# Performance work log

Hardware: AMD Instinct MI355X
Metric: run time of the kernel (lower is better)

The kernel has to match this reference:

```python
import jax, jax.numpy as jnp
import numpy as np
import math

D_MODEL = 1024
H = 16
D_K = D_MODEL // H
SEQ = 4096
NEG = -1000000000.0  # mask constant from the original code


def setup_inputs() -> dict:
    key = jax.random.key(0)
    ks = jax.random.split(key, 7)
    return {
        "Q": jax.random.normal(ks[0], (SEQ, D_MODEL), dtype=jnp.float32),
        "K": jax.random.normal(ks[1], (SEQ, D_MODEL), dtype=jnp.float32),
        "V": jax.random.normal(ks[2], (SEQ, D_MODEL), dtype=jnp.float32),
        "W_Q": jax.random.normal(ks[3], (H, D_MODEL, D_K), dtype=jnp.float32),
        "W_K": jax.random.normal(ks[4], (H, D_MODEL, D_K), dtype=jnp.float32),
        "W_V": jax.random.normal(ks[5], (H, D_MODEL, D_K), dtype=jnp.float32),
        "W_O": jax.random.normal(ks[6], (D_MODEL, D_MODEL), dtype=jnp.float32),
        "mask": 1,
    }


def reference(Q, K, V, W_Q, W_K, W_V, W_O, mask):
    d_k = W_Q.shape[-1]
    s = Q.shape[0]
    # batched per-head projections: [h, s, d_k]
    Qh = jnp.einsum("sd,hdk->hsk", Q, W_Q)
    Kh = jnp.einsum("sd,hdk->hsk", K, W_K)
    Vh = jnp.einsum("sd,hdk->hsk", V, W_V)
    # scores: [h, s_q, s_k]
    scores = jnp.einsum("hqk,hsk->hqs", Qh, Kh) / math.sqrt(d_k)
    if mask:
        # faithful to torch: tril(scores) + triu(ones, 1) * -1e9
        lower = jnp.tril(jnp.ones((s, s), dtype=scores.dtype))
        upper = jnp.triu(jnp.ones((s, s), dtype=scores.dtype), k=1)
        scores = scores * lower + upper * NEG
    attn = jax.nn.softmax(scores, axis=-1)
    heads = jnp.einsum("hqs,hsk->hqk", attn, Vh)  # [h, s, d_k]
    # concat heads along feature dim in head order -> [s, h*d_k]
    concat = jnp.transpose(heads, (1, 0, 2)).reshape(s, -1)
    return concat @ W_O
```

## Files before the change

### kernel.cpp

```cpp
#include <hip/hip_runtime.h>
#include <hip/hip_bf16.h>

constexpr int S      = 4096;
constexpr int DMODEL = 1024;
constexpr int H      = 16;
constexpr int DK     = 64;

typedef __attribute__((ext_vector_type(8))) short          short8;
typedef __attribute__((ext_vector_type(4))) short          short4v;
typedef __attribute__((ext_vector_type(4))) float          float4v;
typedef __attribute__((ext_vector_type(4))) unsigned short ushort4v;
typedef __attribute__((ext_vector_type(8))) unsigned short ushort8;

__device__ __forceinline__ unsigned short f2bf(float x) {
    unsigned u = __builtin_bit_cast(unsigned, x);
    u += 0x7FFFu + ((u >> 16) & 1u);
    return (unsigned short)(u >> 16);
}
__device__ __forceinline__ float bf2f(unsigned short h) {
    unsigned u = ((unsigned)h) << 16;
    return __builtin_bit_cast(float, u);
}
__device__ __forceinline__ float fexp2(float x) { return __builtin_amdgcn_exp2f(x); }

__device__ __forceinline__ void gl_lds16(const unsigned short* g, unsigned short* l) {
    __builtin_amdgcn_global_load_lds(
        (const __attribute__((address_space(1))) unsigned int*)g,
        (__attribute__((address_space(3))) unsigned int*)l, 16, 0, 0);
}

__global__ __launch_bounds__(256) void prep_all(
    const float* __restrict__ Q, const float* __restrict__ K,
    const float* __restrict__ V,
    const float* __restrict__ WQ, const float* __restrict__ WK,
    const float* __restrict__ WV, const float* __restrict__ WO,
    unsigned short* __restrict__ QH, unsigned short* __restrict__ QL,
    unsigned short* __restrict__ KH, unsigned short* __restrict__ KL,
    unsigned short* __restrict__ Vb,
    unsigned short* __restrict__ WqtH, unsigned short* __restrict__ WqtL,
    unsigned short* __restrict__ WktH, unsigned short* __restrict__ WktL,
    unsigned short* __restrict__ Wvt,  unsigned short* __restrict__ WOt)
{
    const int zb = blockIdx.z;
    const int t  = threadIdx.x;

    if (zb < 3) {
        const size_t base = ((size_t)blockIdx.x * 256 + t) * 8;
        const float* src = (zb == 0) ? Q : (zb == 1) ? K : V;
        const float4 a = *(const float4*)(src + base);
        const float4 b = *(const float4*)(src + base + 4);
        const float xs[8] = {a.x, a.y, a.z, a.w, b.x, b.y, b.z, b.w};
        ushort8 hv, lv;
#pragma unroll
        for (int j = 0; j < 8; ++j) {
            const unsigned short h = f2bf(xs[j]);
            hv[j] = h;
            lv[j] = f2bf(xs[j] - bf2f(h));
        }
        if (zb == 0)      { *(ushort8*)(QH + base) = hv; *(ushort8*)(QL + base) = lv; }
        else if (zb == 1) { *(ushort8*)(KH + base) = hv; *(ushort8*)(KL + base) = lv; }
        else              { *(ushort8*)(Vb + base) = hv; }
        return;
    }

    const int bb = blockIdx.x;
    if (bb >= 1024) return;
    const int zfull = bb >> 4;
    const int which = zfull >> 4;
    const int z     = zfull & 15;
    const int r0    = (bb & 15) * 64;

    __shared__ float Ts[64][65];

    const float* in;
    unsigned short *oh, *ol;
    int z_mult, rstride;
    if (which == 0)      { in = WQ; oh = WqtH; ol = WqtL; z_mult = 65536; rstride = 64; }
    else if (which == 1) { in = WK; oh = WktH; ol = WktL; z_mult = 65536; rstride = 64; }
    else if (which == 2) { in = WV; oh = Wvt;  ol = nullptr; z_mult = 65536; rstride = 64; }
    else                 { in = WO; oh = WOt;  ol = nullptr; z_mult = 64;    rstride = 1024; }

    const float* src = in + (size_t)z * z_mult;
#pragma unroll
    for (int i = 0; i < 4; ++i) {
        const int row = (t >> 4) + i * 16;
        const int col = (t & 15) * 4;
        const float4 v = *(const float4*)&src[(size_t)(r0 + row) * rstride + col];
        Ts[row][col + 0] = v.x; Ts[row][col + 1] = v.y;
        Ts[row][col + 2] = v.z; Ts[row][col + 3] = v.w;
    }
    __syncthreads();
#pragma unroll
    for (int i = 0; i < 4; ++i) {
        const int c  = (t >> 4) + i * 16;
        const int rb = (t & 15) * 4;
        ushort4v hv, lv;
#pragma unroll
        for (int j = 0; j < 4; ++j) {
            const float x = Ts[rb + j][c];
            const unsigned short h = f2bf(x);
            hv[j] = h;
            lv[j] = f2bf(x - bf2f(h));
        }
        const size_t o = (size_t)(z * 64 + c) * 1024 + r0 + rb;
        *(ushort4v*)&oh[o] = hv;
        if (ol) *(ushort4v*)&ol[o] = lv;
    }
}

template <bool SPLIT, int EPI>
__device__ __forceinline__ void gemm_core(unsigned short* __restrict__ sm,
                                          const unsigned short* __restrict__ Ah,
                                          const unsigned short* __restrict__ Al,
                                          const unsigned short* __restrict__ Bh,
                                          const unsigned short* __restrict__ Bl,
                                          float* __restrict__ C,
                                          unsigned short* __restrict__ O1,
                                          unsigned short* __restrict__ O2,
                                          int m0, int n0)
{
    unsigned short* AsH = sm;
    unsigned short* BsH = sm + 4096;
    unsigned short* AsL = sm + 8192;
    unsigned short* BsL = sm + 12288;

    const int t    = threadIdx.x;
    const int wave = t >> 6;
    const int lane = t & 63;
    const int quad = lane >> 4;
    const int l15  = lane & 15;
    const int wm   = (wave & 1) * 64;
    const int wn   = (wave >> 1) * 64;

    float4v acc[4][4];
#pragma unroll
    for (int mi = 0; mi < 4; ++mi)
#pragma unroll
        for (int ni = 0; ni < 4; ++ni)
#pragma unroll
            for (int r = 0; r < 4; ++r) acc[mi][ni][r] = 0.f;

    for (int k0 = 0; k0 < 1024; k0 += 32) {
        __syncthreads();
#pragma unroll
        for (int i = 0; i < 2; ++i) {
            const int c   = t + 256 * i;
            const int row = c >> 2;
            const int kc  = (c & 3) * 8;
            const int lb  = (i * 256 + wave * 64) * 8;
            gl_lds16(&Ah[(size_t)(m0 + row) * 1024 + k0 + kc], AsH + lb);
            gl_lds16(&Bh[(size_t)(n0 + row) * 1024 + k0 + kc], BsH + lb);
            if (SPLIT) {
                gl_lds16(&Al[(size_t)(m0 + row) * 1024 + k0 + kc], AsL + lb);
                gl_lds16(&Bl[(size_t)(n0 + row) * 1024 + k0 + kc], BsL + lb);
            }
        }
        __syncthreads();

        short8 afh[4], bfh[4], afl[4], bfl[4];
#pragma unroll
        for (int mi = 0; mi < 4; ++mi)
            afh[mi] = *(const short8*)&AsH[(wm + mi * 16 + l15) * 32 + quad * 8];
#pragma unroll
        for (int ni = 0; ni < 4; ++ni)
            bfh[ni] = *(const short8*)&BsH[(wn + ni * 16 + l15) * 32 + quad * 8];
        if (SPLIT) {
#pragma unroll
            for (int mi = 0; mi < 4; ++mi)
                afl[mi] = *(const short8*)&AsL[(wm + mi * 16 + l15) * 32 + quad * 8];
#pragma unroll
            for (int ni = 0; ni < 4; ++ni)
                bfl[ni] = *(const short8*)&BsL[(wn + ni * 16 + l15) * 32 + quad * 8];
        }

#pragma unroll
        for (int mi = 0; mi < 4; ++mi)
#pragma unroll
            for (int ni = 0; ni < 4; ++ni) {
                acc[mi][ni] = __builtin_amdgcn_mfma_f32_16x16x32_bf16(
                    afh[mi], bfh[ni], acc[mi][ni], 0, 0, 0);
                if (SPLIT) {
                    acc[mi][ni] = __builtin_amdgcn_mfma_f32_16x16x32_bf16(
                        afh[mi], bfl[ni], acc[mi][ni], 0, 0, 0);
                    acc[mi][ni] = __builtin_amdgcn_mfma_f32_16x16x32_bf16(
                        afl[mi], bfh[ni], acc[mi][ni], 0, 0, 0);
                }
            }
    }

    if (EPI == 2) {
        __syncthreads();
        unsigned short* Ts = sm;
#pragma unroll
        for (int mi = 0; mi < 4; ++mi)
#pragma unroll
            for (int ni = 0; ni < 4; ++ni) {
                ushort4v pk;
#pragma unroll
                for (int r = 0; r < 4; ++r) pk[r] = f2bf(acc[mi][ni][r]);
                *(ushort4v*)&Ts[(wn + ni * 16 + l15) * 136 + wm + mi * 16 + quad * 4] = pk;
            }
        __syncthreads();
#pragma unroll
        for (int p = 0; p < 8; ++p) {
            const int n = p * 16 + (t >> 4);
            const int m = (t & 15) * 8;
            *(ushort8*)&O1[(size_t)(n0 + n) * 4096 + m0 + m] =
                *(const ushort8*)&Ts[n * 136 + m];
        }
        return;
    }

#pragma unroll
    for (int mi = 0; mi < 4; ++mi)
#pragma unroll
        for (int r = 0; r < 4; ++r) {
            const int m = m0 + wm + mi * 16 + quad * 4 + r;
            if (EPI == 0) {
                float* cp = C + (size_t)m * 1024 + n0 + wn + l15;
#pragma unroll
                for (int ni = 0; ni < 4; ++ni) cp[ni * 16] = acc[mi][ni][r];
            } else {
                unsigned short* o1 = O1 + (size_t)m * 1024 + n0 + wn + l15;
                unsigned short* o2 = O2 + (size_t)m * 1024 + n0 + wn + l15;
#pragma unroll
                for (int ni = 0; ni < 4; ++ni) {
                    const float v = acc[mi][ni][r];
                    const unsigned short hh = f2bf(v);
                    o1[ni * 16] = hh;
                    o2[ni * 16] = f2bf(v - bf2f(hh));
                }
            }
        }
}

__global__ __launch_bounds__(256) void proj_mfma(
    const unsigned short* __restrict__ XqH, const unsigned short* __restrict__ XqL,
    const unsigned short* __restrict__ XkH, const unsigned short* __restrict__ XkL,
    const unsigned short* __restrict__ Xv,
    const unsigned short* __restrict__ WqtH, const unsigned short* __restrict__ WqtL,
    const unsigned short* __restrict__ WktH, const unsigned short* __restrict__ WktL,
    const unsigned short* __restrict__ Wvt,
    float* __restrict__ Qc,
    unsigned short* __restrict__ KHg, unsigned short* __restrict__ KLg,
    unsigned short* __restrict__ Vt)
{
    __shared__ __align__(16) unsigned short smem[17408];
    const int m0 = blockIdx.x * 128, n0 = blockIdx.y * 128;
    if (blockIdx.z == 0)
        gemm_core<true, 0>(smem, XqH, XqL, WqtH, WqtL, Qc, nullptr, nullptr, m0, n0);
    else if (blockIdx.z == 1)
        gemm_core<true, 1>(smem, XkH, XkL, WktH, WktL, nullptr, KHg, KLg, m0, n0);
    else
        gemm_core<false, 2>(smem, Xv, nullptr, Wvt, nullptr, nullptr, Vt, nullptr, m0, n0);
}

__global__ __launch_bounds__(256) void out_gemm_mfma(
    const unsigned short* __restrict__ Ocb,
    const unsigned short* __restrict__ WOt,
    float* __restrict__ out)
{
    __shared__ __align__(16) unsigned short smem[2 * 4096];
    gemm_core<false, 0>(smem, Ocb, nullptr, WOt, nullptr, out, nullptr, nullptr,
                        blockIdx.x * 128, blockIdx.y * 128);
}

__global__ __launch_bounds__(512) void attn_mfma(const float* __restrict__ Qc,
                                                 const unsigned short* __restrict__ KHg,
                                                 const unsigned short* __restrict__ KLg,
                                                 const unsigned short* __restrict__ Vtg,
                                                 unsigned short* __restrict__ Ocb)
{
    __shared__ __align__(16) short Khi[64][72];
    __shared__ __align__(16) short Klo[64][72];
    __shared__ __align__(16) short Vts[64][72];
    __shared__ __align__(16) short Pb[8][16][72];

    const int bid = blockIdx.x;
    const int h   = bid & 15;
    const int g   = bid >> 4;
    const int qb  = (g < 16) ? (31 - g) : (g - 16);
    const int q0  = qb * 128;
    const int jtmax = 2 * qb + 1;

    const int t    = threadIdx.x;
    const int wave = t >> 6;
    const int lane = t & 63;
    const int quad = lane >> 4;
    const int l15  = lane & 15;

    constexpr float SCL = 0.18033688011112042f;

    short8 qhi[2], qlo[2];
    {
        const int qrow = q0 + wave * 16 + l15;
        const float* qp = Qc + (size_t)qrow * DMODEL + h * 64 + quad * 8;
#pragma unroll
        for (int ks = 0; ks < 2; ++ks) {
            float4 a = *(const float4*)(qp + ks * 32);
            float4 b = *(const float4*)(qp + ks * 32 + 4);
            const float xs[8] = {a.x, a.y, a.z, a.w, b.x, b.y, b.z, b.w};
#pragma unroll
            for (int j = 0; j < 8; ++j) {
                const unsigned short hi = f2bf(xs[j]);
                const unsigned short lo = f2bf(xs[j] - bf2f(hi));
                qhi[ks][j] = (short)hi;
                qlo[ks][j] = (short)lo;
            }
        }
    }

    short8 bones;
    {
        const short ob = (l15 == 0) ? (short)0x3F80 : (short)0;
#pragma unroll
        for (int j = 0; j < 8; ++j) bones[j] = ob;
    }

    float m_r[4] = {-1e30f, -1e30f, -1e30f, -1e30f};
    float4v lacc;
    float4v oacc[4];
#pragma unroll
    for (int r = 0; r < 4; ++r) lacc[r] = 0.f;
#pragma unroll
    for (int nt = 0; nt < 4; ++nt)
#pragma unroll
        for (int r = 0; r < 4; ++r) oacc[nt][r] = 0.f;

    const int srow = t >> 3;
    const int soff = (t & 7) * 8;

    ushort8 kh, kl, vt;
    kh = *(const ushort8*)&KHg[(size_t)srow * 1024 + h * 64 + soff];
    kl = *(const ushort8*)&KLg[(size_t)srow * 1024 + h * 64 + soff];
    vt = *(const ushort8*)&Vtg[(size_t)(h * 64 + srow) * 4096 + soff];

    for (int jt = 0; jt <= jtmax; ++jt) {
        const int j0 = jt * 64;
        *(ushort8*)&Khi[srow][soff] = kh;
        *(ushort8*)&Klo[srow][soff] = kl;
        *(ushort8*)&Vts[srow][soff] = vt;
        __syncthreads();

        if (jt < jtmax) {
            const int jn = j0 + 64;
            kh = *(const ushort8*)&KHg[(size_t)(jn + srow) * 1024 + h * 64 + soff];
            kl = *(const ushort8*)&KLg[(size_t)(jn + srow) * 1024 + h * 64 + soff];
            vt = *(const ushort8*)&Vtg[(size_t)(h * 64 + srow) * 4096 + jn + soff];
        }

        float4v sacc[4];
#pragma unroll
        for (int nt = 0; nt < 4; ++nt)
#pragma unroll
            for (int r = 0; r < 4; ++r) sacc[nt][r] = 0.f;
#pragma unroll
        for (int nt = 0; nt < 4; ++nt) {
            const int key = nt * 16 + l15;
#pragma unroll
            for (int ks = 0; ks < 2; ++ks) {
                const short8 bh = *(const short8*)&Khi[key][ks * 32 + quad * 8];
                const short8 bl = *(const short8*)&Klo[key][ks * 32 + quad * 8];
                sacc[nt] = __builtin_amdgcn_mfma_f32_16x16x32_bf16(qhi[ks], bh, sacc[nt], 0, 0, 0);
                sacc[nt] = __builtin_amdgcn_mfma_f32_16x16x32_bf16(qhi[ks], bl, sacc[nt], 0, 0, 0);
                sacc[nt] = __builtin_amdgcn_mfma_f32_16x16x32_bf16(qlo[ks], bh, sacc[nt], 0, 0, 0);
            }
        }

        if (j0 + 63 > q0 + wave * 16) {
#pragma unroll
            for (int nt = 0; nt < 4; ++nt) {
                const int jg = j0 + nt * 16 + l15;
#pragma unroll
                for (int r = 0; r < 4; ++r) {
                    const int qg = q0 + wave * 16 + quad * 4 + r;
                    const float v = sacc[nt][r] * SCL;
                    sacc[nt][r] = (jg > qg) ? -1e9f : v;
                }
            }
        } else {
#pragma unroll
            for (int nt = 0; nt < 4; ++nt)
#pragma unroll
                for (int r = 0; r < 4; ++r)
                    sacc[nt][r] *= SCL;
        }

        float rmax[4];
#pragma unroll
        for (int r = 0; r < 4; ++r)
            rmax[r] = fmaxf(fmaxf(sacc[0][r], sacc[1][r]), fmaxf(sacc[2][r], sacc[3][r]));
#pragma unroll
        for (int off = 1; off < 16; off <<= 1)
#pragma unroll
            for (int r = 0; r < 4; ++r)
                rmax[r] = fmaxf(rmax[r], __shfl_xor(rmax[r], off));

        float alpha[4];
#pragma unroll
        for (int r = 0; r < 4; ++r) {
            const float mn = fmaxf(m_r[r], rmax[r]);
            alpha[r] = fexp2(m_r[r] - mn);
            m_r[r] = mn;
        }

#pragma unroll
        for (int nt = 0; nt < 4; ++nt)
#pragma unroll
            for (int r = 0; r < 4; ++r)
                sacc[nt][r] = fexp2(sacc[nt][r] - m_r[r]);

#pragma unroll
        for (int r = 0; r < 4; ++r) lacc[r] *= alpha[r];
#pragma unroll
        for (int nt = 0; nt < 4; ++nt)
#pragma unroll
            for (int r = 0; r < 4; ++r)
                oacc[nt][r] *= alpha[r];

#pragma unroll
        for (int nt = 0; nt < 4; ++nt)
#pragma unroll
            for (int r = 0; r < 4; ++r)
                Pb[wave][quad * 4 + r][nt * 16 + l15] = (short)f2bf(sacc[nt][r]);
        __asm__ volatile("s_waitcnt lgkmcnt(0)" ::: "memory");

        short8 af[2];
        af[0] = *(const short8*)&Pb[wave][l15][quad * 8];
        af[1] = *(const short8*)&Pb[wave][l15][32 + quad * 8];
#pragma unroll
        for (int nt = 0; nt < 4; ++nt) {
            const int dk = nt * 16 + l15;
#pragma unroll
            for (int ks = 0; ks < 2; ++ks) {
                const short8 bv = *(const short8*)&Vts[dk][ks * 32 + quad * 8];
                oacc[nt] = __builtin_amdgcn_mfma_f32_16x16x32_bf16(af[ks], bv, oacc[nt], 0, 0, 0);
            }
        }
        lacc = __builtin_amdgcn_mfma_f32_16x16x32_bf16(af[0], bones, lacc, 0, 0, 0);
        lacc = __builtin_amdgcn_mfma_f32_16x16x32_bf16(af[1], bones, lacc, 0, 0, 0);
        __syncthreads();
    }

#pragma unroll
    for (int r = 0; r < 4; ++r) {
        const float lsum = __shfl(lacc[r], (lane & 48));
        const float inv  = 1.0f / lsum;
        const int qg = q0 + wave * 16 + quad * 4 + r;
        unsigned short* op = Ocb + (size_t)qg * DMODEL + h * 64 + l15;
#pragma unroll
        for (int nt = 0; nt < 4; ++nt)
            op[nt * 16] = f2bf(oacc[nt][r] * inv);
    }
}

extern "C" void kernel_launch(void* const* d_in, const int* in_sizes, int n_in,
                              void* d_out, int out_size, void* d_ws, size_t ws_size,
                              hipStream_t stream)
{
    const float* Q  = (const float*)d_in[0];
    const float* K  = (const float*)d_in[1];
    const float* V  = (const float*)d_in[2];
    const float* WQ = (const float*)d_in[3];
    const float* WK = (const float*)d_in[4];
    const float* WV = (const float*)d_in[5];
    const float* WO = (const float*)d_in[6];

    float* out = (float*)d_out;

    const size_t SD4 = (size_t)S * DMODEL * 4;
    const size_t SD2 = (size_t)S * DMODEL * 2;
    const size_t W2  = (size_t)DMODEL * DMODEL * 2;
    char* p = (char*)d_ws;
    auto take = [&](size_t b) { char* r = p; p += b; return r; };

    float* Qc = (float*)take(SD4);
    unsigned short* KHg = (unsigned short*)take(SD2);
    unsigned short* KLg = (unsigned short*)take(SD2);
    unsigned short* Vtg = (unsigned short*)take(SD2);
    unsigned short* XqH = (unsigned short*)take(SD2);
    unsigned short* XqL = (unsigned short*)take(SD2);
    unsigned short* XkH = (unsigned short*)take(SD2);
    unsigned short* XkL = (unsigned short*)take(SD2);
    unsigned short* Xv  = (unsigned short*)take(SD2);
    unsigned short* WqtH = (unsigned short*)take(W2);
    unsigned short* WqtL = (unsigned short*)take(W2);
    unsigned short* WktH = (unsigned short*)take(W2);
    unsigned short* WktL = (unsigned short*)take(W2);
    unsigned short* Wvt  = (unsigned short*)take(W2);
    unsigned short* WOt  = (unsigned short*)take(W2);
    unsigned short* Ocb  = (unsigned short*)take(SD2);

    prep_all<<<dim3(2048, 1, 4), 256, 0, stream>>>(
        Q, K, V, WQ, WK, WV, WO,
        XqH, XqL, XkH, XkL, Xv, WqtH, WqtL, WktH, WktL, Wvt, WOt);
    proj_mfma<<<dim3(S / 128, DMODEL / 128, 3), 256, 0, stream>>>(
        XqH, XqL, XkH, XkL, Xv, WqtH, WqtL, WktH, WktL, Wvt, Qc, KHg, KLg, Vtg);
    attn_mfma<<<dim3((S / 128) * H), 512, 0, stream>>>(Qc, KHg, KLg, Vtg, Ocb);
    out_gemm_mfma<<<dim3(S / 128, DMODEL / 128), 256, 0, stream>>>(Ocb, WOt, out);
}
```

Measured before the change: 332.9 us.

## Skip fully-masked key tiles per wave and defer softmax rescale in attention

Each wave now skips all QK, softmax and PV work for key tiles lying entirely above its 16 query rows, keeping only the shared LDS staging and barriers. Scaling is folded into an fma inside exp2, so the max is taken on unscaled scores. The online-softmax rescale of the accumulators is skipped when no row's max grows anywhere in the wave. P is packed with the hardware v_cvt_pk_bf16_f32 instruction instead of software rounding. This cuts wasted MFMA and exp work on the causal diagonal, at the cost of more wave divergence and a slightly different mask constant.

```diff
diff --git a/kernel.cpp b/kernel.cpp
--- a/kernel.cpp
+++ b/kernel.cpp
@@ -22,6 +22,12 @@
     return __builtin_bit_cast(float, u);
 }
 __device__ __forceinline__ float fexp2(float x) { return __builtin_amdgcn_exp2f(x); }
+
+__device__ __forceinline__ unsigned cvtpk_bf16(float lo, float hi) {
+    unsigned r;
+    asm("v_cvt_pk_bf16_f32 %0, %1, %2" : "=v"(r) : "v"(lo), "v"(hi));
+    return r;
+}
 
 __device__ __forceinline__ void gl_lds16(const unsigned short* g, unsigned short* l) {
     __builtin_amdgcn_global_load_lds(
@@ -335,6 +341,7 @@
     kl = *(const ushort8*)&KLg[(size_t)srow * 1024 + h * 64 + soff];
     vt = *(const ushort8*)&Vtg[(size_t)(h * 64 + srow) * 4096 + soff];
 
+    const int qrow_lo = q0 + wave * 16;
     for (int jt = 0; jt <= jtmax; ++jt) {
         const int j0 = jt * 64;
         *(ushort8*)&Khi[srow][soff] = kh;
@@ -349,96 +356,97 @@
             vt = *(const ushort8*)&Vtg[(size_t)(h * 64 + srow) * 4096 + jn + soff];
         }
 
-        float4v sacc[4];
-#pragma unroll
-        for (int nt = 0; nt < 4; ++nt)
-#pragma unroll
-            for (int r = 0; r < 4; ++r) sacc[nt][r] = 0.f;
-#pragma unroll
-        for (int nt = 0; nt < 4; ++nt) {
-            const int key = nt * 16 + l15;
-#pragma unroll
-            for (int ks = 0; ks < 2; ++ks) {
-                const short8 bh = *(const short8*)&Khi[key][ks * 32 + quad * 8];
-                const short8 bl = *(const short8*)&Klo[key][ks * 32 + quad * 8];
-                sacc[nt] = __builtin_amdgcn_mfma_f32_16x16x32_bf16(qhi[ks], bh, sacc[nt], 0, 0, 0);
-                sacc[nt] = __builtin_amdgcn_mfma_f32_16x16x32_bf16(qhi[ks], bl, sacc[nt], 0, 0, 0);
-                sacc[nt] = __builtin_amdgcn_mfma_f32_16x16x32_bf16(qlo[ks], bh, sacc[nt], 0, 0, 0);
-            }
-        }
-
-        if (j0 + 63 > q0 + wave * 16) {
+        if (j0 <= qrow_lo + 15) {
+            float4v sacc[4];
+#pragma unroll
+            for (int nt = 0; nt < 4; ++nt)
+#pragma unroll
+                for (int r = 0; r < 4; ++r) sacc[nt][r] = 0.f;
 #pragma unroll
             for (int nt = 0; nt < 4; ++nt) {
-                const int jg = j0 + nt * 16 + l15;
+                const int key = nt * 16 + l15;
+#pragma unroll
+                for (int ks = 0; ks < 2; ++ks) {
+                    const short8 bh = *(const short8*)&Khi[key][ks * 32 + quad * 8];
+                    const short8 bl = *(const short8*)&Klo[key][ks * 32 + quad * 8];
+                    sacc[nt] = __builtin_amdgcn_mfma_f32_16x16x32_bf16(qhi[ks], bh, sacc[nt], 0, 0, 0);
+                    sacc[nt] = __builtin_amdgcn_mfma_f32_16x16x32_bf16(qhi[ks], bl, sacc[nt], 0, 0, 0);
+                    sacc[nt] = __builtin_amdgcn_mfma_f32_16x16x32_bf16(qlo[ks], bh, sacc[nt], 0, 0, 0);
+                }
+            }
+
+            if (j0 + 63 > qrow_lo) {
+#pragma unroll
+                for (int nt = 0; nt < 4; ++nt) {
+                    const int jg = j0 + nt * 16 + l15;
+#pragma unroll
+                    for (int r = 0; r < 4; ++r) {
+                        const int qg = qrow_lo + quad * 4 + r;
+                        if (jg > qg) sacc[nt][r] = -1e10f;
+                    }
+                }
+            }
+
+            float rmax[4];
+#pragma unroll
+            for (int r = 0; r < 4; ++r)
+                rmax[r] = fmaxf(fmaxf(sacc[0][r], sacc[1][r]), fmaxf(sacc[2][r], sacc[3][r]));
+#pragma unroll
+            for (int off = 1; off < 16; off <<= 1)
+#pragma unroll
+                for (int r = 0; r < 4; ++r)
+                    rmax[r] = fmaxf(rmax[r], __shfl_xor(rmax[r], off));
+
+            float rs[4];
+#pragma unroll
+            for (int r = 0; r < 4; ++r) rs[r] = rmax[r] * SCL;
+            const bool grow = (rs[0] > m_r[0]) || (rs[1] > m_r[1]) ||
+                              (rs[2] > m_r[2]) || (rs[3] > m_r[3]);
+            if (__any(grow)) {
 #pragma unroll
                 for (int r = 0; r < 4; ++r) {
-                    const int qg = q0 + wave * 16 + quad * 4 + r;
-                    const float v = sacc[nt][r] * SCL;
-                    sacc[nt][r] = (jg > qg) ? -1e9f : v;
-                }
-            }
-        } else {
+                    const float mn   = fmaxf(m_r[r], rs[r]);
+                    const float alpha = fexp2(m_r[r] - mn);
+                    m_r[r] = mn;
+                    lacc[r] *= alpha;
+#pragma unroll
+                    for (int nt = 0; nt < 4; ++nt) oacc[nt][r] *= alpha;
+                }
+            }
+
 #pragma unroll
             for (int nt = 0; nt < 4; ++nt)
 #pragma unroll
                 for (int r = 0; r < 4; ++r)
-                    sacc[nt][r] *= SCL;
-        }
-
-        float rmax[4];
-#pragma unroll
-        for (int r = 0; r < 4; ++r)
-            rmax[r] = fmaxf(fmaxf(sacc[0][r], sacc[1][r]), fmaxf(sacc[2][r], sacc[3][r]));
-#pragma unroll
-        for (int off = 1; off < 16; off <<= 1)
-#pragma unroll
-            for (int r = 0; r < 4; ++r)
-                rmax[r] = fmaxf(rmax[r], __shfl_xor(rmax[r], off));
-
-        float alpha[4];
-#pragma unroll
-        for (int r = 0; r < 4; ++r) {
-            const float mn = fmaxf(m_r[r], rmax[r]);
-            alpha[r] = fexp2(m_r[r] - mn);
-            m_r[r] = mn;
-        }
-
-#pragma unroll
-        for (int nt = 0; nt < 4; ++nt)
-#pragma unroll
-            for (int r = 0; r < 4; ++r)
-                sacc[nt][r] = fexp2(sacc[nt][r] - m_r[r]);
-
-#pragma unroll
-        for (int r = 0; r < 4; ++r) lacc[r] *= alpha[r];
-#pragma unroll
-        for (int nt = 0; nt < 4; ++nt)
-#pragma unroll
-            for (int r = 0; r < 4; ++r)
-                oacc[nt][r] *= alpha[r];
-
-#pragma unroll
-        for (int nt = 0; nt < 4; ++nt)
-#pragma unroll
-            for (int r = 0; r < 4; ++r)
-                Pb[wave][quad * 4 + r][nt * 16 + l15] = (short)f2bf(sacc[nt][r]);
-        __asm__ volatile("s_waitcnt lgkmcnt(0)" ::: "memory");
-
-        short8 af[2];
-        af[0] = *(const short8*)&Pb[wave][l15][quad * 8];
-        af[1] = *(const short8*)&Pb[wave][l15][32 + quad * 8];
-#pragma unroll
-        for (int nt = 0; nt < 4; ++nt) {
-            const int dk = nt * 16 + l15;
-#pragma unroll
-            for (int ks = 0; ks < 2; ++ks) {
-                const short8 bv = *(const short8*)&Vts[dk][ks * 32 + quad * 8];
-                oacc[nt] = __builtin_amdgcn_mfma_f32_16x16x32_bf16(af[ks], bv, oacc[nt], 0, 0, 0);
-            }
-        }
-        lacc = __builtin_amdgcn_mfma_f32_16x16x32_bf16(af[0], bones, lacc, 0, 0, 0);
-        lacc = __builtin_amdgcn_mfma_f32_16x16x32_bf16(af[1], bones, lacc, 0, 0, 0);
+                    sacc[nt][r] = fexp2(__builtin_fmaf(sacc[nt][r], SCL, -m_r[r]));
+
+#pragma unroll
+            for (int r = 0; r < 4; ++r) {
+                const int prow = quad * 4 + r;
+#pragma unroll
+                for (int np = 0; np < 2; ++np) {
+                    const unsigned w = cvtpk_bf16(sacc[2 * np][r], sacc[2 * np + 1][r]);
+                    Pb[wave][prow][(2 * np) * 16 + l15]     = (short)(w & 0xffffu);
+                    Pb[wave][prow][(2 * np + 1) * 16 + l15] = (short)(w >> 16);
+                }
+            }
+            __asm__ volatile("s_waitcnt lgkmcnt(0)" ::: "memory");
+
+            short8 af[2];
+            af[0] = *(const short8*)&Pb[wave][l15][quad * 8];
+            af[1] = *(const short8*)&Pb[wave][l15][32 + quad * 8];
+#pragma unroll
+            for (int nt = 0; nt < 4; ++nt) {
+                const int dk = nt * 16 + l15;
+#pragma unroll
+                for (int ks = 0; ks < 2; ++ks) {
+                    const short8 bv = *(const short8*)&Vts[dk][ks * 32 + quad * 8];
+                    oacc[nt] = __builtin_amdgcn_mfma_f32_16x16x32_bf16(af[ks], bv, oacc[nt], 0, 0, 0);
+                }
+            }
+            lacc = __builtin_amdgcn_mfma_f32_16x16x32_bf16(af[0], bones, lacc, 0, 0, 0);
+            lacc = __builtin_amdgcn_mfma_f32_16x16x32_bf16(af[1], bones, lacc, 0, 0, 0);
+        }
         __syncthreads();
     }
 
```

Result: no change. 328.1 us (-1.4%).
